# Performance work log

Hardware: AMD Instinct MI355X
Metric: run time of the kernel (lower is better)

Reference implementation:

```python
import jax, jax.numpy as jnp
import numpy as np

ALPHA = 0.2  # LeakyReLU negative slope


def setup_inputs() -> dict:
    key = jax.random.key(0)
    k1, k2, k3, k4 = jax.random.split(key, 4)
    B, N, F_IN, F_OUT = 8, 2048, 512, 256
    h = jax.random.normal(k1, (B, N, F_IN), dtype=jnp.float32)
    # torch nn.Linear weights: [out, in]
    W = jax.random.normal(k2, (F_OUT, F_IN), dtype=jnp.float32) * (1.414 / np.sqrt(F_IN))
    a1 = jax.random.normal(k3, (1, F_OUT), dtype=jnp.float32) * (1.414 / np.sqrt(F_OUT))
    a2 = jax.random.normal(k4, (1, F_OUT), dtype=jnp.float32) * (1.414 / np.sqrt(F_OUT))
    return {"h": h, "W": W, "a1": a1, "a2": a2}


def reference(h, W, a1, a2):
    # Wh: [B, N, F_out]
    Wh = jnp.einsum('bnf,of->bno', h, W)
    # additive attention scores
    s1 = jnp.einsum('bno,o->bn', Wh, a1[0])  # [B, N]
    s2 = jnp.einsum('bno,o->bn', Wh, a2[0])  # [B, N]
    e = s1[:, :, None] + s2[:, None, :]       # [B, N, N]
    e = jnp.where(e > 0, e, ALPHA * e)         # LeakyReLU
    attention = jax.nn.softmax(e, axis=2)      # softmax over last dim
    # dropout p=0.0 -> identity
    h_prime = jnp.einsum('bnm,bmo->bno', attention, Wh)
    return jax.nn.elu(h_prime)  # concat=True path
```

## Files before the change

### kernel.cpp

```cpp
#include <hip/hip_runtime.h>

typedef __attribute__((ext_vector_type(8))) _Float16 half8;
typedef __attribute__((ext_vector_type(4))) _Float16 half4;
typedef __attribute__((ext_vector_type(4))) float f32x4;
#if __has_builtin(__builtin_amdgcn_cvt_pkrtz)
typedef __attribute__((ext_vector_type(2))) __fp16 fp16x2;
#endif

#define ALPHA 0.2f
#define LOG2E 1.44269504f

__device__ __forceinline__ void gload_lds16(const void* g, void* l) {
  __builtin_amdgcn_global_load_lds((const __attribute__((address_space(1))) unsigned int*)g,
                                   (__attribute__((address_space(3))) unsigned int*)l, 16, 0, 0);
}

__device__ __forceinline__ float fexp2(float x) {
#if __has_builtin(__builtin_amdgcn_exp2f)
  return __builtin_amdgcn_exp2f(x);
#else
  return exp2f(x);
#endif
}

__global__ __launch_bounds__(256) void k_convW(const float* __restrict__ W,
                                               _Float16* __restrict__ W16) {
  int idx4 = blockIdx.x * 256 + threadIdx.x;
  int n = idx4 >> 7;
  int q = idx4 & 127;
  float4 v = *reinterpret_cast<const float4*>(W + n * 512 + q * 4);
  half4 hv = {(_Float16)v.x, (_Float16)v.y, (_Float16)v.z, (_Float16)v.w};
  int kp = (q * 4) ^ ((n & 7) << 3);
  *reinterpret_cast<half4*>(W16 + n * 512 + kp) = hv;
}

__global__ __launch_bounds__(256) void k_uvec(const float* __restrict__ W,
                                              const float* __restrict__ a1,
                                              const float* __restrict__ a2,
                                              float* __restrict__ u1,
                                              float* __restrict__ u2) {
  __shared__ float p1[4][64], p2[4][64];
  int t = threadIdx.x;
  int l = t & 63, g = t >> 6;
  int k = blockIdx.x * 64 + l;
  float x1 = 0.f, x2 = 0.f;
  for (int o = g * 64; o < g * 64 + 64; ++o) {
    float wv = W[o * 512 + k];
    x1 += wv * a1[o];
    x2 += wv * a2[o];
  }
  p1[g][l] = x1; p2[g][l] = x2;
  __syncthreads();
  if (g == 0) {
    u1[k] = p1[0][l] + p1[1][l] + p1[2][l] + p1[3][l];
    u2[k] = p2[0][l] + p2[1][l] + p2[2][l] + p2[3][l];
  }
}

__global__ __launch_bounds__(256) void k_gemm_wh(const float* __restrict__ h,
                                                 const _Float16* __restrict__ W16,
                                                 const float* __restrict__ u1,
                                                 const float* __restrict__ u2,
                                                 float* __restrict__ s1o,
                                                 float* __restrict__ s2o,
                                                 _Float16* __restrict__ WhT) {
  __shared__ _Float16 Ab[2][32 * 64];
  __shared__ _Float16 Bb[2][256 * 64];
  const int t = threadIdx.x, lane = t & 63, w = t >> 6;
  const int i0 = blockIdx.x * 32;
  const int b = i0 >> 11, n0 = i0 & 2047;
  const int ar = t >> 3, au = t & 7;
  const float* hrow = h + (size_t)(i0 + ar) * 512 + au * 8;

  f32x4 acc[2][4];
#pragma unroll
  for (int mi = 0; mi < 2; ++mi)
#pragma unroll
    for (int ni = 0; ni < 4; ++ni) acc[mi][ni] = (f32x4){0.f, 0.f, 0.f, 0.f};

  float4 aR0 = *reinterpret_cast<const float4*>(hrow);
  float4 aR1 = *reinterpret_cast<const float4*>(hrow + 4);
#pragma unroll
  for (int q = 0; q < 8; ++q) {
    int idx = (q * 4 + w) * 64 + lane;
    int nn = idx >> 3, uu = idx & 7;
    gload_lds16(W16 + nn * 512 + uu * 8, (char*)&Bb[0][0] + idx * 16);
  }
  float x1 = 0.f, x2 = 0.f;

  for (int kt = 0; kt < 8; ++kt) {
    const int cur = kt & 1;
    {
      half8 av;
      av[0] = (_Float16)aR0.x; av[1] = (_Float16)aR0.y;
      av[2] = (_Float16)aR0.z; av[3] = (_Float16)aR0.w;
      av[4] = (_Float16)aR1.x; av[5] = (_Float16)aR1.y;
      av[6] = (_Float16)aR1.z; av[7] = (_Float16)aR1.w;
      *reinterpret_cast<half8*>((char*)&Ab[cur][0] + ar * 128 + ((au * 16) ^ ((ar & 7) << 4))) = av;
      const float* up1 = u1 + kt * 64 + au * 8;
      const float* up2 = u2 + kt * 64 + au * 8;
      float4 u1a = *reinterpret_cast<const float4*>(up1);
      float4 u1b = *reinterpret_cast<const float4*>(up1 + 4);
      float4 u2a = *reinterpret_cast<const float4*>(up2);
      float4 u2b = *reinterpret_cast<const float4*>(up2 + 4);
      x1 += aR0.x * u1a.x + aR0.y * u1a.y + aR0.z * u1a.z + aR0.w * u1a.w
          + aR1.x * u1b.x + aR1.y * u1b.y + aR1.z * u1b.z + aR1.w * u1b.w;
      x2 += aR0.x * u2a.x + aR0.y * u2a.y + aR0.z * u2a.z + aR0.w * u2a.w
          + aR1.x * u2b.x + aR1.y * u2b.y + aR1.z * u2b.z + aR1.w * u2b.w;
    }
    __syncthreads();
    if (kt < 7) {
      const int k0 = (kt + 1) * 64;
      aR0 = *reinterpret_cast<const float4*>(hrow + k0);
      aR1 = *reinterpret_cast<const float4*>(hrow + k0 + 4);
#pragma unroll
      for (int q = 0; q < 8; ++q) {
        int idx = (q * 4 + w) * 64 + lane;
        int nn = idx >> 3, uu = idx & 7;
        gload_lds16(W16 + nn * 512 + k0 + uu * 8, (char*)&Bb[cur ^ 1][0] + idx * 16);
      }
    }
    const char* Ac = (const char*)&Ab[cur][0];
    const char* Bc = (const char*)&Bb[cur][0];
#pragma unroll
    for (int kk = 0; kk < 2; ++kk) {
      const int jb = (lane >> 4) * 16 + kk * 64;
      half8 afr[2];
#pragma unroll
      for (int mi = 0; mi < 2; ++mi) {
        int rr = (lane & 15) + 16 * mi;
        afr[mi] = *reinterpret_cast<const half8*>(Ac + rr * 128 + (jb ^ ((rr & 7) << 4)));
      }
#pragma unroll
      for (int ni = 0; ni < 4; ++ni) {
        int nn = 64 * w + 16 * ni + (lane & 15);
        half8 bfr = *reinterpret_cast<const half8*>(Bc + nn * 128 + (jb ^ ((nn & 7) << 4)));
#pragma unroll
        for (int mi = 0; mi < 2; ++mi)
          acc[mi][ni] = __builtin_amdgcn_mfma_f32_16x16x32_f16(afr[mi], bfr, acc[mi][ni], 0, 0, 0);
      }
    }
  }
  x1 += __shfl_xor(x1, 1); x1 += __shfl_xor(x1, 2); x1 += __shfl_xor(x1, 4);
  x2 += __shfl_xor(x2, 1); x2 += __shfl_xor(x2, 2); x2 += __shfl_xor(x2, 4);
  if (au == 0) { s1o[i0 + ar] = x1; s2o[i0 + ar] = x2; }
  _Float16* whtb = WhT + (size_t)b * 256 * 2048;
#pragma unroll
  for (int mi = 0; mi < 2; ++mi)
#pragma unroll
    for (int ni = 0; ni < 4; ++ni) {
      int c = 64 * w + 16 * ni + (lane & 15);
      int nb = n0 + 16 * mi + (lane >> 4) * 4;
      int np = nb ^ ((c & 7) << 3);
      f32x4 a = acc[mi][ni];
      half4 hv = {(_Float16)a[0], (_Float16)a[1], (_Float16)a[2], (_Float16)a[3]};
      *reinterpret_cast<half4*>(whtb + (size_t)c * 2048 + np) = hv;
    }
}

__global__ __launch_bounds__(1024) void k_attn(const _Float16* __restrict__ WhT,
                                               const float* __restrict__ s1,
                                               const float* __restrict__ s2,
                                               float* __restrict__ out) {
  __shared__ _Float16 Bb[3][256 * 64];
  __shared__ _Float16 Pb[2][64 * 64];
  __shared__ float s2s[2048];
  __shared__ float red[16];
  __shared__ float d_lds[64];
  const int t = threadIdx.x, lane = t & 63, w = t >> 6;
  const int rg = w >> 2, cg = w & 3;
  const int b = blockIdx.x & 7;
  const int i0 = (blockIdx.x >> 3) * 64;
  const _Float16* whtb = WhT + (size_t)b * 256 * 2048;
  const int arow = lane & 15;
  const int pr = t >> 4, pj = t & 15;
  const float s1v = s1[b * 2048 + i0 + pr];

  float2 sv2 = *reinterpret_cast<const float2*>(s2 + b * 2048 + t * 2);
  float m0 = fmaxf(sv2.x, sv2.y);
  *reinterpret_cast<float2*>(&s2s[t * 2]) = make_float2(sv2.x * LOG2E, sv2.y * LOG2E);
#pragma unroll
  for (int off = 32; off >= 1; off >>= 1) m0 = fmaxf(m0, __shfl_xor(m0, off));
  if (lane == 0) red[w] = m0;
  __syncthreads();
  float smaxL;
  {
    float mm = red[0];
#pragma unroll
    for (int i = 1; i < 16; ++i) mm = fmaxf(mm, red[i]);
    smaxL = mm * LOG2E;
  }
  const float s1L = LOG2E * s1v;
  const float e0L = s1L + smaxL;
  const float mrowL = fmaxf(e0L, ALPHA * e0L);
  const float C1 = s1L - mrowL;
  const float C2 = fmaf(ALPHA, s1L, -mrowL);
  const int pwoff = pr * 128 + ((pj * 8) ^ ((pr & 7) << 4));
  half8 onesb;
  {
    _Float16 ov = (arow == 0) ? (_Float16)1.0f : (_Float16)0.0f;
#pragma unroll
    for (int x = 0; x < 8; ++x) onesb[x] = ov;
  }
  f32x4 acc[4];
#pragma unroll
  for (int ni = 0; ni < 4; ++ni) acc[ni] = (f32x4){0.f, 0.f, 0.f, 0.f};
  f32x4 accd = (f32x4){0.f, 0.f, 0.f, 0.f};

  {
    float4 sv = *reinterpret_cast<const float4*>(&s2s[pj * 4]);
    float p0 = fexp2(fmaxf(C1 + sv.x, fmaf(ALPHA, sv.x, C2)));
    float p1 = fexp2(fmaxf(C1 + sv.y, fmaf(ALPHA, sv.y, C2)));
    float p2 = fexp2(fmaxf(C1 + sv.z, fmaf(ALPHA, sv.z, C2)));
    float p3 = fexp2(fmaxf(C1 + sv.w, fmaf(ALPHA, sv.w, C2)));
    half4 hv;
#if __has_builtin(__builtin_amdgcn_cvt_pkrtz)
    fp16x2 q0 = __builtin_amdgcn_cvt_pkrtz(p0, p1);
    fp16x2 q1 = __builtin_amdgcn_cvt_pkrtz(p2, p3);
    hv[0] = (_Float16)q0[0]; hv[1] = (_Float16)q0[1];
    hv[2] = (_Float16)q1[0]; hv[3] = (_Float16)q1[1];
#else
    hv[0] = (_Float16)p0; hv[1] = (_Float16)p1; hv[2] = (_Float16)p2; hv[3] = (_Float16)p3;
#endif
    *reinterpret_cast<half4*>((char*)&Pb[0][0] + pwoff) = hv;
  }
#pragma unroll
  for (int x = 0; x < 2; ++x)
#pragma unroll
    for (int q = 0; q < 2; ++q) {
      int idx = q * 1024 + t;
      int cl = idx >> 3, uu = idx & 7;
      gload_lds16(whtb + (size_t)cl * 2048 + x * 64 + uu * 8, (char*)&Bb[x][0] + idx * 16);
    }

  for (int jt = 0; jt < 32; ++jt) {
    if (jt < 31) asm volatile("s_waitcnt vmcnt(2) lgkmcnt(0)" ::: "memory");
    else         asm volatile("s_waitcnt vmcnt(0) lgkmcnt(0)" ::: "memory");
    __builtin_amdgcn_s_barrier();
    if (jt < 30) {
      const int j0n = (jt + 2) * 64;
      const int p = (jt + 2) % 3;
#pragma unroll
      for (int q = 0; q < 2; ++q) {
        int idx = q * 1024 + t;
        int cl = idx >> 3, uu = idx & 7;
        gload_lds16(whtb + (size_t)cl * 2048 + j0n + uu * 8, (char*)&Bb[p][0] + idx * 16);
      }
    }
    if (jt < 31) {
      float4 sv = *reinterpret_cast<const float4*>(&s2s[(jt + 1) * 64 + pj * 4]);
      float p0 = fexp2(fmaxf(C1 + sv.x, fmaf(ALPHA, sv.x, C2)));
      float p1 = fexp2(fmaxf(C1 + sv.y, fmaf(ALPHA, sv.y, C2)));
      float p2 = fexp2(fmaxf(C1 + sv.z, fmaf(ALPHA, sv.z, C2)));
      float p3 = fexp2(fmaxf(C1 + sv.w, fmaf(ALPHA, sv.w, C2)));
      half4 hv;
#if __has_builtin(__builtin_amdgcn_cvt_pkrtz)
      fp16x2 q0 = __builtin_amdgcn_cvt_pkrtz(p0, p1);
      fp16x2 q1 = __builtin_amdgcn_cvt_pkrtz(p2, p3);
      hv[0] = (_Float16)q0[0]; hv[1] = (_Float16)q0[1];
      hv[2] = (_Float16)q1[0]; hv[3] = (_Float16)q1[1];
#else
      hv[0] = (_Float16)p0; hv[1] = (_Float16)p1; hv[2] = (_Float16)p2; hv[3] = (_Float16)p3;
#endif
      *reinterpret_cast<half4*>((char*)&Pb[(jt + 1) & 1][0] + pwoff) = hv;
    }
    const char* Bc = (const char*)&Bb[jt % 3][0];
    const char* Pc = (const char*)&Pb[jt & 1][0];
#pragma unroll
    for (int kk = 0; kk < 2; ++kk) {
      const int jb = ((lane >> 4) * 8 + kk * 32) * 2;
      const int ar64 = rg * 16 + arow;
      half8 afr = *reinterpret_cast<const half8*>(Pc + ar64 * 128 + (jb ^ ((ar64 & 7) << 4)));
      if (cg == 0)
        accd = __builtin_amdgcn_mfma_f32_16x16x32_f16(afr, onesb, accd, 0, 0, 0);
#pragma unroll
      for (int ni = 0; ni < 4; ++ni) {
        int cl = cg * 64 + 16 * ni + arow;
        half8 bfr = *reinterpret_cast<const half8*>(Bc + cl * 128 + (jb ^ ((cl & 7) << 4)));
        acc[ni] = __builtin_amdgcn_mfma_f32_16x16x32_f16(afr, bfr, acc[ni], 0, 0, 0);
      }
    }
  }
  if (cg == 0 && arow == 0) {
#pragma unroll
    for (int reg = 0; reg < 4; ++reg)
      d_lds[rg * 16 + (lane >> 4) * 4 + reg] = accd[reg];
  }
  __syncthreads();
  const size_t ob = ((size_t)b * 2048 + i0 + rg * 16) * 256 + cg * 64;
#pragma unroll
  for (int reg = 0; reg < 4; ++reg) {
    int rr = (lane >> 4) * 4 + reg;
    float inv = 1.0f / d_lds[rg * 16 + rr];
#pragma unroll
    for (int ni = 0; ni < 4; ++ni) {
      int c = 16 * ni + arow;
      float v = acc[ni][reg] * inv;
      v = v > 0.f ? v : (__expf(v) - 1.f);
      out[ob + (size_t)rr * 256 + c] = v;
    }
  }
}

extern "C" void kernel_launch(void* const* d_in, const int* in_sizes, int n_in,
                              void* d_out, int out_size, void* d_ws, size_t ws_size,
                              hipStream_t stream) {
  (void)in_sizes; (void)n_in; (void)out_size; (void)ws_size;
  const float* h = (const float*)d_in[0];
  const float* W = (const float*)d_in[1];
  const float* a1 = (const float*)d_in[2];
  const float* a2 = (const float*)d_in[3];
  float* out = (float*)d_out;
  char* ws = (char*)d_ws;
  _Float16* WhT = (_Float16*)(ws);
  _Float16* W16 = (_Float16*)(ws + 8388608);
  float* u1 = (float*)(ws + 8650752);
  float* u2 = (float*)(ws + 8652800);
  float* s1 = (float*)(ws + 8654848);
  float* s2 = (float*)(ws + 8720384);

  hipLaunchKernelGGL(k_convW, dim3(128), dim3(256), 0, stream, W, W16);
  hipLaunchKernelGGL(k_uvec, dim3(8), dim3(256), 0, stream, W, a1, a2, u1, u2);
  hipLaunchKernelGGL(k_gemm_wh, dim3(512), dim3(256), 0, stream, h, W16, u1, u2, s1, s2, WhT);
  hipLaunchKernelGGL(k_attn, dim3(256), dim3(1024), 0, stream, WhT, s1, s2, out);
}
```

Baseline: 72.66 us.

## Compute attention probabilities in registers and halve attention block size

The attention kernel now uses 512 threads, and each wave covers 32 query rows instead of 16. Each wave builds its MFMA A-fragments directly in registers from s2 and the exp2 formula, so the P tile no longer goes through LDS. Row sums are accumulated in scalar registers instead of through an extra MFMA against a ones vector. The B buffer drops from triple to double buffering, which needs a second barrier before refilling. Each B fragment load now feeds two MFMAs, but the exp work per wave is duplicated across the column-group waves and occupancy per block changes.

```diff
diff --git a/kernel.cpp b/kernel.cpp
--- a/kernel.cpp
+++ b/kernel.cpp
@@ -158,146 +158,148 @@
     }
 }
 
-__global__ __launch_bounds__(1024) void k_attn(const _Float16* __restrict__ WhT,
-                                               const float* __restrict__ s1,
-                                               const float* __restrict__ s2,
-                                               float* __restrict__ out) {
-  __shared__ _Float16 Bb[3][256 * 64];
-  __shared__ _Float16 Pb[2][64 * 64];
+#if __has_builtin(__builtin_amdgcn_cvt_pkrtz)
+#define PACK2(DST, I, A, B)                        \
+  { fp16x2 q_ = __builtin_amdgcn_cvt_pkrtz(A, B);  \
+    DST[I] = (_Float16)q_[0]; DST[I + 1] = (_Float16)q_[1]; }
+#else
+#define PACK2(DST, I, A, B) { DST[I] = (_Float16)(A); DST[I + 1] = (_Float16)(B); }
+#endif
+
+#define EXP8(OUT, V0, V1, C1_, C2_, DS)                               \
+  {                                                                   \
+    float p0 = fexp2(fmaxf(C1_ + V0.x, fmaf(ALPHA, V0.x, C2_)));      \
+    float p1 = fexp2(fmaxf(C1_ + V0.y, fmaf(ALPHA, V0.y, C2_)));      \
+    float p2 = fexp2(fmaxf(C1_ + V0.z, fmaf(ALPHA, V0.z, C2_)));      \
+    float p3 = fexp2(fmaxf(C1_ + V0.w, fmaf(ALPHA, V0.w, C2_)));      \
+    float p4 = fexp2(fmaxf(C1_ + V1.x, fmaf(ALPHA, V1.x, C2_)));      \
+    float p5 = fexp2(fmaxf(C1_ + V1.y, fmaf(ALPHA, V1.y, C2_)));      \
+    float p6 = fexp2(fmaxf(C1_ + V1.z, fmaf(ALPHA, V1.z, C2_)));      \
+    float p7 = fexp2(fmaxf(C1_ + V1.w, fmaf(ALPHA, V1.w, C2_)));      \
+    DS += ((p0 + p1) + (p2 + p3)) + ((p4 + p5) + (p6 + p7));          \
+    PACK2(OUT, 0, p0, p1); PACK2(OUT, 2, p2, p3);                     \
+    PACK2(OUT, 4, p4, p5); PACK2(OUT, 6, p6, p7);                     \
+  }
+
+__global__ __launch_bounds__(512) void k_attn(const _Float16* __restrict__ WhT,
+                                              const float* __restrict__ s1,
+                                              const float* __restrict__ s2,
+                                              float* __restrict__ out) {
+  __shared__ _Float16 Bb[2][256 * 64];
   __shared__ float s2s[2048];
-  __shared__ float red[16];
-  __shared__ float d_lds[64];
+  __shared__ float red[8];
   const int t = threadIdx.x, lane = t & 63, w = t >> 6;
   const int rg = w >> 2, cg = w & 3;
   const int b = blockIdx.x & 7;
   const int i0 = (blockIdx.x >> 3) * 64;
   const _Float16* whtb = WhT + (size_t)b * 256 * 2048;
   const int arow = lane & 15;
-  const int pr = t >> 4, pj = t & 15;
-  const float s1v = s1[b * 2048 + i0 + pr];
-
-  float2 sv2 = *reinterpret_cast<const float2*>(s2 + b * 2048 + t * 2);
-  float m0 = fmaxf(sv2.x, sv2.y);
-  *reinterpret_cast<float2*>(&s2s[t * 2]) = make_float2(sv2.x * LOG2E, sv2.y * LOG2E);
+
+  float4 sv4 = *reinterpret_cast<const float4*>(s2 + b * 2048 + t * 4);
+  float m0 = fmaxf(fmaxf(sv4.x, sv4.y), fmaxf(sv4.z, sv4.w));
+  *reinterpret_cast<float4*>(&s2s[t * 4]) =
+      make_float4(sv4.x * LOG2E, sv4.y * LOG2E, sv4.z * LOG2E, sv4.w * LOG2E);
 #pragma unroll
   for (int off = 32; off >= 1; off >>= 1) m0 = fmaxf(m0, __shfl_xor(m0, off));
   if (lane == 0) red[w] = m0;
+  const float s1A = s1[b * 2048 + i0 + rg * 32 + arow];
+  const float s1B = s1[b * 2048 + i0 + rg * 32 + 16 + arow];
   __syncthreads();
   float smaxL;
   {
-    float mm = red[0];
-#pragma unroll
-    for (int i = 1; i < 16; ++i) mm = fmaxf(mm, red[i]);
+    float mm = fmaxf(fmaxf(red[0], red[1]), fmaxf(red[2], red[3]));
+    mm = fmaxf(mm, fmaxf(fmaxf(red[4], red[5]), fmaxf(red[6], red[7])));
     smaxL = mm * LOG2E;
   }
-  const float s1L = LOG2E * s1v;
-  const float e0L = s1L + smaxL;
-  const float mrowL = fmaxf(e0L, ALPHA * e0L);
-  const float C1 = s1L - mrowL;
-  const float C2 = fmaf(ALPHA, s1L, -mrowL);
-  const int pwoff = pr * 128 + ((pj * 8) ^ ((pr & 7) << 4));
-  half8 onesb;
-  {
-    _Float16 ov = (arow == 0) ? (_Float16)1.0f : (_Float16)0.0f;
-#pragma unroll
-    for (int x = 0; x < 8; ++x) onesb[x] = ov;
-  }
-  f32x4 acc[4];
-#pragma unroll
-  for (int ni = 0; ni < 4; ++ni) acc[ni] = (f32x4){0.f, 0.f, 0.f, 0.f};
-  f32x4 accd = (f32x4){0.f, 0.f, 0.f, 0.f};
-
-  {
-    float4 sv = *reinterpret_cast<const float4*>(&s2s[pj * 4]);
-    float p0 = fexp2(fmaxf(C1 + sv.x, fmaf(ALPHA, sv.x, C2)));
-    float p1 = fexp2(fmaxf(C1 + sv.y, fmaf(ALPHA, sv.y, C2)));
-    float p2 = fexp2(fmaxf(C1 + sv.z, fmaf(ALPHA, sv.z, C2)));
-    float p3 = fexp2(fmaxf(C1 + sv.w, fmaf(ALPHA, sv.w, C2)));
-    half4 hv;
-#if __has_builtin(__builtin_amdgcn_cvt_pkrtz)
-    fp16x2 q0 = __builtin_amdgcn_cvt_pkrtz(p0, p1);
-    fp16x2 q1 = __builtin_amdgcn_cvt_pkrtz(p2, p3);
-    hv[0] = (_Float16)q0[0]; hv[1] = (_Float16)q0[1];
-    hv[2] = (_Float16)q1[0]; hv[3] = (_Float16)q1[1];
-#else
-    hv[0] = (_Float16)p0; hv[1] = (_Float16)p1; hv[2] = (_Float16)p2; hv[3] = (_Float16)p3;
-#endif
-    *reinterpret_cast<half4*>((char*)&Pb[0][0] + pwoff) = hv;
-  }
+  const float s1LA = LOG2E * s1A;
+  const float eA = s1LA + smaxL;
+  const float mA = fmaxf(eA, ALPHA * eA);
+  const float C1A = s1LA - mA;
+  const float C2A = fmaf(ALPHA, s1LA, -mA);
+  const float s1LB = LOG2E * s1B;
+  const float eB = s1LB + smaxL;
+  const float mB = fmaxf(eB, ALPHA * eB);
+  const float C1B = s1LB - mB;
+  const float C2B = fmaf(ALPHA, s1LB, -mB);
+
+  f32x4 acc[2][4];
+#pragma unroll
+  for (int mi = 0; mi < 2; ++mi)
+#pragma unroll
+    for (int ni = 0; ni < 4; ++ni) acc[mi][ni] = (f32x4){0.f, 0.f, 0.f, 0.f};
+  float dsA = 0.f, dsB = 0.f;
+
 #pragma unroll
   for (int x = 0; x < 2; ++x)
 #pragma unroll
-    for (int q = 0; q < 2; ++q) {
-      int idx = q * 1024 + t;
+    for (int q = 0; q < 4; ++q) {
+      int idx = q * 512 + t;
       int cl = idx >> 3, uu = idx & 7;
       gload_lds16(whtb + (size_t)cl * 2048 + x * 64 + uu * 8, (char*)&Bb[x][0] + idx * 16);
     }
 
+  const int js = (lane >> 4) * 8;
+#pragma unroll 1
   for (int jt = 0; jt < 32; ++jt) {
-    if (jt < 31) asm volatile("s_waitcnt vmcnt(2) lgkmcnt(0)" ::: "memory");
-    else         asm volatile("s_waitcnt vmcnt(0) lgkmcnt(0)" ::: "memory");
+    if (jt < 31) asm volatile("s_waitcnt vmcnt(4)" ::: "memory");
+    else         asm volatile("s_waitcnt vmcnt(0)" ::: "memory");
+    __builtin_amdgcn_s_barrier();
+    const char* Bc = (const char*)&Bb[jt & 1][0];
+    const float* sp = &s2s[jt * 64 + js];
+    float4 v00 = *reinterpret_cast<const float4*>(sp);
+    float4 v01 = *reinterpret_cast<const float4*>(sp + 4);
+    float4 v10 = *reinterpret_cast<const float4*>(sp + 32);
+    float4 v11 = *reinterpret_cast<const float4*>(sp + 36);
+    half8 afrA0, afrA1, afrB0, afrB1;
+    EXP8(afrA0, v00, v01, C1A, C2A, dsA);
+    EXP8(afrA1, v10, v11, C1A, C2A, dsA);
+    EXP8(afrB0, v00, v01, C1B, C2B, dsB);
+    EXP8(afrB1, v10, v11, C1B, C2B, dsB);
+#pragma unroll
+    for (int kk = 0; kk < 2; ++kk) {
+      const int jb = (lane >> 4) * 16 + kk * 64;
+#pragma unroll
+      for (int ni = 0; ni < 4; ++ni) {
+        int cl = cg * 64 + 16 * ni + arow;
+        half8 bfr = *reinterpret_cast<const half8*>(Bc + cl * 128 + (jb ^ ((cl & 7) << 4)));
+        acc[0][ni] = __builtin_amdgcn_mfma_f32_16x16x32_f16(kk ? afrA1 : afrA0, bfr, acc[0][ni], 0, 0, 0);
+        acc[1][ni] = __builtin_amdgcn_mfma_f32_16x16x32_f16(kk ? afrB1 : afrB0, bfr, acc[1][ni], 0, 0, 0);
+      }
+    }
+    asm volatile("" ::: "memory");
     __builtin_amdgcn_s_barrier();
     if (jt < 30) {
       const int j0n = (jt + 2) * 64;
-      const int p = (jt + 2) % 3;
-#pragma unroll
-      for (int q = 0; q < 2; ++q) {
-        int idx = q * 1024 + t;
+#pragma unroll
+      for (int q = 0; q < 4; ++q) {
+        int idx = q * 512 + t;
         int cl = idx >> 3, uu = idx & 7;
-        gload_lds16(whtb + (size_t)cl * 2048 + j0n + uu * 8, (char*)&Bb[p][0] + idx * 16);
-      }
-    }
-    if (jt < 31) {
-      float4 sv = *reinterpret_cast<const float4*>(&s2s[(jt + 1) * 64 + pj * 4]);
-      float p0 = fexp2(fmaxf(C1 + sv.x, fmaf(ALPHA, sv.x, C2)));
-      float p1 = fexp2(fmaxf(C1 + sv.y, fmaf(ALPHA, sv.y, C2)));
-      float p2 = fexp2(fmaxf(C1 + sv.z, fmaf(ALPHA, sv.z, C2)));
-      float p3 = fexp2(fmaxf(C1 + sv.w, fmaf(ALPHA, sv.w, C2)));
-      half4 hv;
-#if __has_builtin(__builtin_amdgcn_cvt_pkrtz)
-      fp16x2 q0 = __builtin_amdgcn_cvt_pkrtz(p0, p1);
-      fp16x2 q1 = __builtin_amdgcn_cvt_pkrtz(p2, p3);
-      hv[0] = (_Float16)q0[0]; hv[1] = (_Float16)q0[1];
-      hv[2] = (_Float16)q1[0]; hv[3] = (_Float16)q1[1];
-#else
-      hv[0] = (_Float16)p0; hv[1] = (_Float16)p1; hv[2] = (_Float16)p2; hv[3] = (_Float16)p3;
-#endif
-      *reinterpret_cast<half4*>((char*)&Pb[(jt + 1) & 1][0] + pwoff) = hv;
-    }
-    const char* Bc = (const char*)&Bb[jt % 3][0];
-    const char* Pc = (const char*)&Pb[jt & 1][0];
-#pragma unroll
-    for (int kk = 0; kk < 2; ++kk) {
-      const int jb = ((lane >> 4) * 8 + kk * 32) * 2;
-      const int ar64 = rg * 16 + arow;
-      half8 afr = *reinterpret_cast<const half8*>(Pc + ar64 * 128 + (jb ^ ((ar64 & 7) << 4)));
-      if (cg == 0)
-        accd = __builtin_amdgcn_mfma_f32_16x16x32_f16(afr, onesb, accd, 0, 0, 0);
-#pragma unroll
-      for (int ni = 0; ni < 4; ++ni) {
-        int cl = cg * 64 + 16 * ni + arow;
-        half8 bfr = *reinterpret_cast<const half8*>(Bc + cl * 128 + (jb ^ ((cl & 7) << 4)));
-        acc[ni] = __builtin_amdgcn_mfma_f32_16x16x32_f16(afr, bfr, acc[ni], 0, 0, 0);
-      }
-    }
-  }
-  if (cg == 0 && arow == 0) {
-#pragma unroll
-    for (int reg = 0; reg < 4; ++reg)
-      d_lds[rg * 16 + (lane >> 4) * 4 + reg] = accd[reg];
-  }
-  __syncthreads();
-  const size_t ob = ((size_t)b * 2048 + i0 + rg * 16) * 256 + cg * 64;
+        gload_lds16(whtb + (size_t)cl * 2048 + j0n + uu * 8, (char*)&Bb[jt & 1][0] + idx * 16);
+      }
+    }
+  }
+
+  dsA += __shfl_xor(dsA, 16); dsA += __shfl_xor(dsA, 32);
+  dsB += __shfl_xor(dsB, 16); dsB += __shfl_xor(dsB, 32);
+  float invA[4], invB[4];
 #pragma unroll
   for (int reg = 0; reg < 4; ++reg) {
     int rr = (lane >> 4) * 4 + reg;
-    float inv = 1.0f / d_lds[rg * 16 + rr];
+    invA[reg] = 1.0f / __shfl(dsA, rr);
+    invB[reg] = 1.0f / __shfl(dsB, rr);
+  }
+  const size_t ob = ((size_t)b * 2048 + i0 + rg * 32 + (lane >> 4) * 4) * 256 + cg * 64;
+#pragma unroll
+  for (int reg = 0; reg < 4; ++reg) {
 #pragma unroll
     for (int ni = 0; ni < 4; ++ni) {
       int c = 16 * ni + arow;
-      float v = acc[ni][reg] * inv;
-      v = v > 0.f ? v : (__expf(v) - 1.f);
-      out[ob + (size_t)rr * 256 + c] = v;
+      float v0 = acc[0][ni][reg] * invA[reg];
+      v0 = v0 > 0.f ? v0 : (__expf(v0) - 1.f);
+      out[ob + (size_t)reg * 256 + c] = v0;
+      float v1 = acc[1][ni][reg] * invB[reg];
+      v1 = v1 > 0.f ? v1 : (__expf(v1) - 1.f);
+      out[ob + (size_t)(16 + reg) * 256 + c] = v1;
     }
   }
 }
@@ -322,5 +324,5 @@
   hipLaunchKernelGGL(k_convW, dim3(128), dim3(256), 0, stream, W, W16);
   hipLaunchKernelGGL(k_uvec, dim3(8), dim3(256), 0, stream, W, a1, a2, u1, u2);
   hipLaunchKernelGGL(k_gemm_wh, dim3(512), dim3(256), 0, stream, h, W16, u1, u2, s1, s2, WhT);
-  hipLaunchKernelGGL(k_attn, dim3(256), dim3(1024), 0, stream, WhT, s1, s2, out);
-}
+  hipLaunchKernelGGL(k_attn, dim3(256), dim3(512), 0, stream, WhT, s1, s2, out);
+}
```

After: 87.42 us. 1.2x slower.

## Split attention output columns across blocks and merge prologue kernels

Applied to the files above, without the earlier changes.

The attention kernel now splits the 256 output features into two halves handled by separate blocks of 512 threads. This doubles the grid to 512 blocks and halves the per-block LDS staging buffer, so more blocks can be resident across the CUs. Each block still recomputes the full softmax probabilities for its rows, so the exp work is duplicated across the two halves. Separately, the W conversion and u-vector kernels are fused into one launch to save a kernel launch.

```diff
diff --git a/kernel.cpp b/kernel.cpp
--- a/kernel.cpp
+++ b/kernel.cpp
@@ -23,37 +23,59 @@
 #endif
 }
 
-__global__ __launch_bounds__(256) void k_convW(const float* __restrict__ W,
-                                               _Float16* __restrict__ W16) {
-  int idx4 = blockIdx.x * 256 + threadIdx.x;
-  int n = idx4 >> 7;
-  int q = idx4 & 127;
-  float4 v = *reinterpret_cast<const float4*>(W + n * 512 + q * 4);
-  half4 hv = {(_Float16)v.x, (_Float16)v.y, (_Float16)v.z, (_Float16)v.w};
-  int kp = (q * 4) ^ ((n & 7) << 3);
-  *reinterpret_cast<half4*>(W16 + n * 512 + kp) = hv;
-}
-
-__global__ __launch_bounds__(256) void k_uvec(const float* __restrict__ W,
-                                              const float* __restrict__ a1,
-                                              const float* __restrict__ a2,
-                                              float* __restrict__ u1,
-                                              float* __restrict__ u2) {
-  __shared__ float p1[4][64], p2[4][64];
-  int t = threadIdx.x;
-  int l = t & 63, g = t >> 6;
-  int k = blockIdx.x * 64 + l;
-  float x1 = 0.f, x2 = 0.f;
-  for (int o = g * 64; o < g * 64 + 64; ++o) {
-    float wv = W[o * 512 + k];
-    x1 += wv * a1[o];
-    x2 += wv * a2[o];
-  }
-  p1[g][l] = x1; p2[g][l] = x2;
-  __syncthreads();
-  if (g == 0) {
-    u1[k] = p1[0][l] + p1[1][l] + p1[2][l] + p1[3][l];
-    u2[k] = p2[0][l] + p2[1][l] + p2[2][l] + p2[3][l];
+#if __has_builtin(__builtin_amdgcn_cvt_pkrtz)
+#define PACK2(DST, I, A, B)                        \
+  { fp16x2 q_ = __builtin_amdgcn_cvt_pkrtz(A, B);  \
+    DST[I] = (_Float16)q_[0]; DST[I + 1] = (_Float16)q_[1]; }
+#else
+#define PACK2(DST, I, A, B) { DST[I] = (_Float16)(A); DST[I + 1] = (_Float16)(B); }
+#endif
+
+#define EXP8(OUT, V0, V1, C1_, C2_)                                   \
+  {                                                                   \
+    float p0 = fexp2(fmaxf(C1_ + V0.x, fmaf(ALPHA, V0.x, C2_)));      \
+    float p1 = fexp2(fmaxf(C1_ + V0.y, fmaf(ALPHA, V0.y, C2_)));      \
+    float p2 = fexp2(fmaxf(C1_ + V0.z, fmaf(ALPHA, V0.z, C2_)));      \
+    float p3 = fexp2(fmaxf(C1_ + V0.w, fmaf(ALPHA, V0.w, C2_)));      \
+    float p4 = fexp2(fmaxf(C1_ + V1.x, fmaf(ALPHA, V1.x, C2_)));      \
+    float p5 = fexp2(fmaxf(C1_ + V1.y, fmaf(ALPHA, V1.y, C2_)));      \
+    float p6 = fexp2(fmaxf(C1_ + V1.z, fmaf(ALPHA, V1.z, C2_)));      \
+    float p7 = fexp2(fmaxf(C1_ + V1.w, fmaf(ALPHA, V1.w, C2_)));      \
+    PACK2(OUT, 0, p0, p1); PACK2(OUT, 2, p2, p3);                     \
+    PACK2(OUT, 4, p4, p5); PACK2(OUT, 6, p6, p7);                     \
+  }
+
+__global__ __launch_bounds__(256) void k_prologue(const float* __restrict__ W,
+                                                  const float* __restrict__ a1,
+                                                  const float* __restrict__ a2,
+                                                  _Float16* __restrict__ W16,
+                                                  float* __restrict__ u1,
+                                                  float* __restrict__ u2) {
+  const int bid = blockIdx.x, t = threadIdx.x;
+  if (bid < 128) {
+    int idx4 = bid * 256 + t;
+    int n = idx4 >> 7;
+    int q = idx4 & 127;
+    float4 v = *reinterpret_cast<const float4*>(W + n * 512 + q * 4);
+    half4 hv = {(_Float16)v.x, (_Float16)v.y, (_Float16)v.z, (_Float16)v.w};
+    int kp = (q * 4) ^ ((n & 7) << 3);
+    *reinterpret_cast<half4*>(W16 + n * 512 + kp) = hv;
+  } else {
+    __shared__ float p1[4][64], p2[4][64];
+    int l = t & 63, g = t >> 6;
+    int k = (bid - 128) * 64 + l;
+    float x1 = 0.f, x2 = 0.f;
+    for (int o = g * 64; o < g * 64 + 64; ++o) {
+      float wv = W[o * 512 + k];
+      x1 += wv * a1[o];
+      x2 += wv * a2[o];
+    }
+    p1[g][l] = x1; p2[g][l] = x2;
+    __syncthreads();
+    if (g == 0) {
+      u1[k] = p1[0][l] + p1[1][l] + p1[2][l] + p1[3][l];
+      u2[k] = p2[0][l] + p2[1][l] + p2[2][l] + p2[3][l];
+    }
   }
 }
 
@@ -158,36 +180,37 @@
     }
 }
 
-__global__ __launch_bounds__(1024) void k_attn(const _Float16* __restrict__ WhT,
-                                               const float* __restrict__ s1,
-                                               const float* __restrict__ s2,
-                                               float* __restrict__ out) {
-  __shared__ _Float16 Bb[3][256 * 64];
+__global__ __launch_bounds__(512) void k_attn(const _Float16* __restrict__ WhT,
+                                              const float* __restrict__ s1,
+                                              const float* __restrict__ s2,
+                                              float* __restrict__ out) {
+  __shared__ _Float16 Bb[3][128 * 64];
   __shared__ _Float16 Pb[2][64 * 64];
   __shared__ float s2s[2048];
-  __shared__ float red[16];
+  __shared__ float red[8];
   __shared__ float d_lds[64];
   const int t = threadIdx.x, lane = t & 63, w = t >> 6;
-  const int rg = w >> 2, cg = w & 3;
+  const int rg = w >> 1, cg = w & 1;
   const int b = blockIdx.x & 7;
-  const int i0 = (blockIdx.x >> 3) * 64;
-  const _Float16* whtb = WhT + (size_t)b * 256 * 2048;
+  const int i0 = ((blockIdx.x >> 3) & 31) * 64;
+  const int ch = blockIdx.x >> 8;
+  const _Float16* whtb = WhT + ((size_t)b * 256 + ch * 128) * 2048;
   const int arow = lane & 15;
-  const int pr = t >> 4, pj = t & 15;
+  const int pr = t >> 3, pj8 = t & 7;
   const float s1v = s1[b * 2048 + i0 + pr];
 
-  float2 sv2 = *reinterpret_cast<const float2*>(s2 + b * 2048 + t * 2);
-  float m0 = fmaxf(sv2.x, sv2.y);
-  *reinterpret_cast<float2*>(&s2s[t * 2]) = make_float2(sv2.x * LOG2E, sv2.y * LOG2E);
+  float4 sv4 = *reinterpret_cast<const float4*>(s2 + b * 2048 + t * 4);
+  float m0 = fmaxf(fmaxf(sv4.x, sv4.y), fmaxf(sv4.z, sv4.w));
+  *reinterpret_cast<float4*>(&s2s[t * 4]) =
+      make_float4(sv4.x * LOG2E, sv4.y * LOG2E, sv4.z * LOG2E, sv4.w * LOG2E);
 #pragma unroll
   for (int off = 32; off >= 1; off >>= 1) m0 = fmaxf(m0, __shfl_xor(m0, off));
   if (lane == 0) red[w] = m0;
   __syncthreads();
   float smaxL;
   {
-    float mm = red[0];
-#pragma unroll
-    for (int i = 1; i < 16; ++i) mm = fmaxf(mm, red[i]);
+    float mm = fmaxf(fmaxf(red[0], red[1]), fmaxf(red[2], red[3]));
+    mm = fmaxf(mm, fmaxf(fmaxf(red[4], red[5]), fmaxf(red[6], red[7])));
     smaxL = mm * LOG2E;
   }
   const float s1L = LOG2E * s1v;
@@ -195,7 +218,7 @@
   const float mrowL = fmaxf(e0L, ALPHA * e0L);
   const float C1 = s1L - mrowL;
   const float C2 = fmaf(ALPHA, s1L, -mrowL);
-  const int pwoff = pr * 128 + ((pj * 8) ^ ((pr & 7) << 4));
+  const int pwoff = pr * 128 + ((pj8 * 16) ^ ((pr & 7) << 4));
   half8 onesb;
   {
     _Float16 ov = (arow == 0) ? (_Float16)1.0f : (_Float16)0.0f;
@@ -208,27 +231,18 @@
   f32x4 accd = (f32x4){0.f, 0.f, 0.f, 0.f};
 
   {
-    float4 sv = *reinterpret_cast<const float4*>(&s2s[pj * 4]);
-    float p0 = fexp2(fmaxf(C1 + sv.x, fmaf(ALPHA, sv.x, C2)));
-    float p1 = fexp2(fmaxf(C1 + sv.y, fmaf(ALPHA, sv.y, C2)));
-    float p2 = fexp2(fmaxf(C1 + sv.z, fmaf(ALPHA, sv.z, C2)));
-    float p3 = fexp2(fmaxf(C1 + sv.w, fmaf(ALPHA, sv.w, C2)));
-    half4 hv;
-#if __has_builtin(__builtin_amdgcn_cvt_pkrtz)
-    fp16x2 q0 = __builtin_amdgcn_cvt_pkrtz(p0, p1);
-    fp16x2 q1 = __builtin_amdgcn_cvt_pkrtz(p2, p3);
-    hv[0] = (_Float16)q0[0]; hv[1] = (_Float16)q0[1];
-    hv[2] = (_Float16)q1[0]; hv[3] = (_Float16)q1[1];
-#else
-    hv[0] = (_Float16)p0; hv[1] = (_Float16)p1; hv[2] = (_Float16)p2; hv[3] = (_Float16)p3;
-#endif
-    *reinterpret_cast<half4*>((char*)&Pb[0][0] + pwoff) = hv;
+    const float* sp = &s2s[pj8 * 8];
+    float4 v0 = *reinterpret_cast<const float4*>(sp);
+    float4 v1 = *reinterpret_cast<const float4*>(sp + 4);
+    half8 ph;
+    EXP8(ph, v0, v1, C1, C2);
+    *reinterpret_cast<half8*>((char*)&Pb[0][0] + pwoff) = ph;
   }
 #pragma unroll
   for (int x = 0; x < 2; ++x)
 #pragma unroll
     for (int q = 0; q < 2; ++q) {
-      int idx = q * 1024 + t;
+      int idx = q * 512 + t;
       int cl = idx >> 3, uu = idx & 7;
       gload_lds16(whtb + (size_t)cl * 2048 + x * 64 + uu * 8, (char*)&Bb[x][0] + idx * 16);
     }
@@ -242,27 +256,18 @@
       const int p = (jt + 2) % 3;
 #pragma unroll
       for (int q = 0; q < 2; ++q) {
-        int idx = q * 1024 + t;
+        int idx = q * 512 + t;
         int cl = idx >> 3, uu = idx & 7;
         gload_lds16(whtb + (size_t)cl * 2048 + j0n + uu * 8, (char*)&Bb[p][0] + idx * 16);
       }
     }
     if (jt < 31) {
-      float4 sv = *reinterpret_cast<const float4*>(&s2s[(jt + 1) * 64 + pj * 4]);
-      float p0 = fexp2(fmaxf(C1 + sv.x, fmaf(ALPHA, sv.x, C2)));
-      float p1 = fexp2(fmaxf(C1 + sv.y, fmaf(ALPHA, sv.y, C2)));
-      float p2 = fexp2(fmaxf(C1 + sv.z, fmaf(ALPHA, sv.z, C2)));
-      float p3 = fexp2(fmaxf(C1 + sv.w, fmaf(ALPHA, sv.w, C2)));
-      half4 hv;
-#if __has_builtin(__builtin_amdgcn_cvt_pkrtz)
-      fp16x2 q0 = __builtin_amdgcn_cvt_pkrtz(p0, p1);
-      fp16x2 q1 = __builtin_amdgcn_cvt_pkrtz(p2, p3);
-      hv[0] = (_Float16)q0[0]; hv[1] = (_Float16)q0[1];
-      hv[2] = (_Float16)q1[0]; hv[3] = (_Float16)q1[1];
-#else
-      hv[0] = (_Float16)p0; hv[1] = (_Float16)p1; hv[2] = (_Float16)p2; hv[3] = (_Float16)p3;
-#endif
-      *reinterpret_cast<half4*>((char*)&Pb[(jt + 1) & 1][0] + pwoff) = hv;
+      const float* sp = &s2s[(jt + 1) * 64 + pj8 * 8];
+      float4 v0 = *reinterpret_cast<const float4*>(sp);
+      float4 v1 = *reinterpret_cast<const float4*>(sp + 4);
+      half8 ph;
+      EXP8(ph, v0, v1, C1, C2);
+      *reinterpret_cast<half8*>((char*)&Pb[(jt + 1) & 1][0] + pwoff) = ph;
     }
     const char* Bc = (const char*)&Bb[jt % 3][0];
     const char* Pc = (const char*)&Pb[jt & 1][0];
@@ -287,7 +292,7 @@
       d_lds[rg * 16 + (lane >> 4) * 4 + reg] = accd[reg];
   }
   __syncthreads();
-  const size_t ob = ((size_t)b * 2048 + i0 + rg * 16) * 256 + cg * 64;
+  const size_t ob = ((size_t)b * 2048 + i0 + rg * 16) * 256 + ch * 128 + cg * 64;
 #pragma unroll
   for (int reg = 0; reg < 4; ++reg) {
     int rr = (lane >> 4) * 4 + reg;
@@ -319,8 +324,7 @@
   float* s1 = (float*)(ws + 8654848);
   float* s2 = (float*)(ws + 8720384);
 
-  hipLaunchKernelGGL(k_convW, dim3(128), dim3(256), 0, stream, W, W16);
-  hipLaunchKernelGGL(k_uvec, dim3(8), dim3(256), 0, stream, W, a1, a2, u1, u2);
+  hipLaunchKernelGGL(k_prologue, dim3(136), dim3(256), 0, stream, W, a1, a2, W16, u1, u2);
   hipLaunchKernelGGL(k_gemm_wh, dim3(512), dim3(256), 0, stream, h, W16, u1, u2, s1, s2, WhT);
-  hipLaunchKernelGGL(k_attn, dim3(256), dim3(1024), 0, stream, WhT, s1, s2, out);
-}
+  hipLaunchKernelGGL(k_attn, dim3(512), dim3(512), 0, stream, WhT, s1, s2, out);
+}
```

Result: faster. 67.07 us (-7.7%).
